# Kernel optimization log

Measured on AMD Instinct MI355X. Metric: run time of the kernel, lower is better.

## Reference

```python
import jax, jax.numpy as jnp
import numpy as np

N, P, Q, T, J, B, H = 262144, 64, 64, 2048, 512, 8, 64


def setup_inputs() -> dict:
    key = jax.random.key(0)
    ks = jax.random.split(key, 11)
    sH = 1.0 / np.sqrt(H).astype(np.float32)
    return {
        "idx": jax.random.randint(ks[0], (B,), 0, J),
        "seg_ids": jnp.sort(jax.random.randint(ks[1], (N,), 0, T)),
        "K": jax.random.normal(ks[2], (N, P), jnp.float32) * 0.1,
        "V": jax.random.normal(ks[3], (N, Q), jnp.float32),
        "S": jax.random.normal(ks[4], (P, J), jnp.float32) * 0.1,
        "W_ih": jax.random.normal(ks[5], (3 * H, Q), jnp.float32) * sH,
        "W_hh": jax.random.normal(ks[6], (3 * H, H), jnp.float32) * sH,
        "b_ih": jax.random.normal(ks[7], (3 * H,), jnp.float32) * sH,
        "b_hh": jax.random.normal(ks[8], (3 * H,), jnp.float32) * sH,
        "w_out": jax.random.normal(ks[9], (1, H), jnp.float32) * sH,
        "b_out": jax.random.normal(ks[10], (1,), jnp.float32) * sH,
    }


def reference(idx, seg_ids, K, V, S, W_ih, W_hh, b_ih, b_hh, w_out, b_out):
    # W[:, b] = K @ S[:, idx[b]]  -> [N, B]
    w = K @ S[:, idx]
    # ragged per-segment softmax over the N axis (segments = date windows)
    m = jax.ops.segment_max(w, seg_ids, num_segments=T)          # [T, B]
    e = jnp.exp(w - m[seg_ids])                                  # [N, B]
    denom = jax.ops.segment_sum(e, seg_ids, num_segments=T)     # [T, B]
    alpha = e / denom[seg_ids]                                   # [N, B]
    # weighted aggregation of V rows per segment: M[t, b] = sum_u alpha_u * V_u
    M = jax.ops.segment_sum(alpha[:, :, None] * V[:, None, :],
                            seg_ids, num_segments=T)             # [T, B, Q]
    X = jnp.transpose(M, (1, 0, 2))                              # [B, T, Q]

    # PyTorch GRU (gate order r,z,n). Faithful to the original bug: GRU was
    # built without batch_first=True, so axis 0 (B) is time, axis 1 (T) is batch.
    def step(h, x_t):  # x_t: [T, Q], h: [T, H]
        gi = x_t @ W_ih.T + b_ih                                 # [T, 3H]
        gh = h @ W_hh.T + b_hh                                   # [T, 3H]
        i_r, i_z, i_n = jnp.split(gi, 3, axis=1)
        h_r, h_z, h_n = jnp.split(gh, 3, axis=1)
        r = jax.nn.sigmoid(i_r + h_r)
        z = jax.nn.sigmoid(i_z + h_z)
        n = jnp.tanh(i_n + r * h_n)
        h_new = (1.0 - z) * n + z * h
        return h_new, h_new

    h0 = jnp.zeros((T, H), X.dtype)
    _, hs = jax.lax.scan(step, h0, X)                            # [B, T, H]
    preds = hs @ w_out.T + b_out                                 # [B, T, 1]
    return preds
```

## Files before the change

### kernel.cpp

```cpp
#include <hip/hip_runtime.h>
#include <math.h>

#define NN 262144
#define PP 64
#define QQ 64
#define TT 2048
#define JJ 512
#define BB 8
#define HH 64

__device__ __forceinline__ float lane_bcast(float v, int l) {
  return __int_as_float(__builtin_amdgcn_readlane(__float_as_int(v), l));
}

__global__ void k_prep(const int* __restrict__ seg_ids, const int* __restrict__ idx,
                       const float* __restrict__ S, int* __restrict__ seg_start,
                       float* __restrict__ s_cols) {
  int tid = blockIdx.x * blockDim.x + threadIdx.x;
  if (tid <= TT) {
    int lo = 0, hi = NN;
    while (lo < hi) {
      int mid = (lo + hi) >> 1;
      int v = seg_ids[mid];
      if (v < tid) lo = mid + 1; else hi = mid;
    }
    seg_start[tid] = lo;
  }
  int t2 = tid - (TT + 1);
  if (t2 >= 0 && t2 < PP * BB) {
    int p = t2 >> 3, b = t2 & 7;
    s_cols[b * PP + p] = S[p * JJ + idx[b]];
  }
}

__global__ __launch_bounds__(256) void k_w(const float* __restrict__ Kmat,
                                           const float* __restrict__ s_cols,
                                           float* __restrict__ ew) {
  __shared__ __align__(16) float s_lds[BB * PP];
  int tid = threadIdx.x;
  for (int i = tid; i < BB * PP; i += 256) s_lds[i] = s_cols[i];
  __syncthreads();
  int n = blockIdx.x * 64 + (tid >> 2);
  int sub = tid & 3;
  const float4* Kp = reinterpret_cast<const float4*>(Kmat + (size_t)n * PP + sub * 16);
  float4 kq[4];
#pragma unroll
  for (int j = 0; j < 4; ++j) kq[j] = Kp[j];
  float acc[8];
#pragma unroll
  for (int b = 0; b < 8; ++b) acc[b] = 0.f;
#pragma unroll
  for (int j4 = 0; j4 < 4; ++j4) {
    float4 kk = kq[j4];
#pragma unroll
    for (int b = 0; b < 8; ++b) {
      const float4 sv = *reinterpret_cast<const float4*>(&s_lds[b * PP + sub * 16 + j4 * 4]);
      acc[b] += kk.x * sv.x + kk.y * sv.y + kk.z * sv.z + kk.w * sv.w;
    }
  }
#pragma unroll
  for (int b = 0; b < 8; ++b) {
    acc[b] += __shfl_xor(acc[b], 1);
    acc[b] += __shfl_xor(acc[b], 2);
  }
  float ox = (sub == 0) ? acc[0] : (sub == 1) ? acc[2] : (sub == 2) ? acc[4] : acc[6];
  float oy = (sub == 0) ? acc[1] : (sub == 1) ? acc[3] : (sub == 2) ? acc[5] : acc[7];
  reinterpret_cast<float2*>(ew + (size_t)n * 8)[sub] =
      make_float2(__expf(ox), __expf(oy));
}

__global__ __launch_bounds__(256) void k_seg(const float* __restrict__ ew,
                                             const float* __restrict__ V,
                                             const int* __restrict__ seg_start,
                                             float* __restrict__ M) {
  int lane = threadIdx.x & 63, wv = threadIdx.x >> 6;
  int t = blockIdx.x * 4 + wv;
  int s = seg_start[t], e = seg_start[t + 1];
  int rsub = lane >> 4;
  int qg = lane & 15;

  float4 acc[8];
#pragma unroll
  for (int b = 0; b < 8; ++b) acc[b] = make_float4(0.f, 0.f, 0.f, 0.f);
  float4 selo = make_float4(0.f, 0.f, 0.f, 0.f);
  float4 sehi = make_float4(0.f, 0.f, 0.f, 0.f);

  int nq = (e - s + 3) >> 2;
  for (int i = 0; i < nq; ++i) {
    int r = s + i * 4 + rsub;
    if (r < e) {
      const float4* ewp = reinterpret_cast<const float4*>(ew + (size_t)r * 8);
      float4 elo = ewp[0], ehi = ewp[1];
      float4 vv = reinterpret_cast<const float4*>(V + (size_t)r * QQ)[qg];
      selo.x += elo.x; selo.y += elo.y; selo.z += elo.z; selo.w += elo.w;
      sehi.x += ehi.x; sehi.y += ehi.y; sehi.z += ehi.z; sehi.w += ehi.w;
      acc[0].x += elo.x * vv.x; acc[0].y += elo.x * vv.y; acc[0].z += elo.x * vv.z; acc[0].w += elo.x * vv.w;
      acc[1].x += elo.y * vv.x; acc[1].y += elo.y * vv.y; acc[1].z += elo.y * vv.z; acc[1].w += elo.y * vv.w;
      acc[2].x += elo.z * vv.x; acc[2].y += elo.z * vv.y; acc[2].z += elo.z * vv.z; acc[2].w += elo.z * vv.w;
      acc[3].x += elo.w * vv.x; acc[3].y += elo.w * vv.y; acc[3].z += elo.w * vv.z; acc[3].w += elo.w * vv.w;
      acc[4].x += ehi.x * vv.x; acc[4].y += ehi.x * vv.y; acc[4].z += ehi.x * vv.z; acc[4].w += ehi.x * vv.w;
      acc[5].x += ehi.y * vv.x; acc[5].y += ehi.y * vv.y; acc[5].z += ehi.y * vv.z; acc[5].w += ehi.y * vv.w;
      acc[6].x += ehi.z * vv.x; acc[6].y += ehi.z * vv.y; acc[6].z += ehi.z * vv.z; acc[6].w += ehi.z * vv.w;
      acc[7].x += ehi.w * vv.x; acc[7].y += ehi.w * vv.y; acc[7].z += ehi.w * vv.z; acc[7].w += ehi.w * vv.w;
    }
  }

#pragma unroll
  for (int b = 0; b < 8; ++b) {
    acc[b].x += __shfl_xor(acc[b].x, 16); acc[b].y += __shfl_xor(acc[b].y, 16);
    acc[b].z += __shfl_xor(acc[b].z, 16); acc[b].w += __shfl_xor(acc[b].w, 16);
    acc[b].x += __shfl_xor(acc[b].x, 32); acc[b].y += __shfl_xor(acc[b].y, 32);
    acc[b].z += __shfl_xor(acc[b].z, 32); acc[b].w += __shfl_xor(acc[b].w, 32);
  }
  selo.x += __shfl_xor(selo.x, 16); selo.y += __shfl_xor(selo.y, 16);
  selo.z += __shfl_xor(selo.z, 16); selo.w += __shfl_xor(selo.w, 16);
  sehi.x += __shfl_xor(sehi.x, 16); sehi.y += __shfl_xor(sehi.y, 16);
  sehi.z += __shfl_xor(sehi.z, 16); sehi.w += __shfl_xor(sehi.w, 16);
  selo.x += __shfl_xor(selo.x, 32); selo.y += __shfl_xor(selo.y, 32);
  selo.z += __shfl_xor(selo.z, 32); selo.w += __shfl_xor(selo.w, 32);
  sehi.x += __shfl_xor(sehi.x, 32); sehi.y += __shfl_xor(sehi.y, 32);
  sehi.z += __shfl_xor(sehi.z, 32); sehi.w += __shfl_xor(sehi.w, 32);

  if (rsub == 0) {
    float inv[8];
    inv[0] = (selo.x > 0.f) ? 1.f / selo.x : 0.f;
    inv[1] = (selo.y > 0.f) ? 1.f / selo.y : 0.f;
    inv[2] = (selo.z > 0.f) ? 1.f / selo.z : 0.f;
    inv[3] = (selo.w > 0.f) ? 1.f / selo.w : 0.f;
    inv[4] = (sehi.x > 0.f) ? 1.f / sehi.x : 0.f;
    inv[5] = (sehi.y > 0.f) ? 1.f / sehi.y : 0.f;
    inv[6] = (sehi.z > 0.f) ? 1.f / sehi.z : 0.f;
    inv[7] = (sehi.w > 0.f) ? 1.f / sehi.w : 0.f;
#pragma unroll
    for (int b = 0; b < 8; ++b) {
      float4 o = make_float4(acc[b].x * inv[b], acc[b].y * inv[b],
                             acc[b].z * inv[b], acc[b].w * inv[b]);
      *reinterpret_cast<float4*>(M + (size_t)t * 512 + b * 64 + qg * 4) = o;
    }
  }
}

__global__ __launch_bounds__(256) void k_gi(const float* __restrict__ M,
                                            const float* __restrict__ W_ih,
                                            const float* __restrict__ b_ih,
                                            float* __restrict__ GI) {
  __shared__ float Wt[64 * 193];
  int tid = threadIdx.x;
  for (int i = tid; i < 192 * 64; i += 256) {
    int g = i >> 6, k = i & 63;
    Wt[k * 193 + g] = W_ih[i];
  }
  __syncthreads();
  int lane = tid & 63, wv = tid >> 6;
  int row0 = blockIdx.x * 32 + wv * 8;
  float x[8];
#pragma unroll
  for (int rr = 0; rr < 8; ++rr) {
    int rho = row0 + rr;
    int b = rho >> 11, t = rho & 2047;
    x[rr] = M[((size_t)t * 8 + b) * 64 + lane];
  }
  float bi0 = b_ih[lane], bi1 = b_ih[64 + lane], bi2 = b_ih[128 + lane];
  float a0[8], a1[8], a2[8];
#pragma unroll
  for (int rr = 0; rr < 8; ++rr) { a0[rr] = bi0; a1[rr] = bi1; a2[rr] = bi2; }
#pragma unroll
  for (int k = 0; k < 64; ++k) {
    float w0 = Wt[k * 193 + lane];
    float w1 = Wt[k * 193 + 64 + lane];
    float w2 = Wt[k * 193 + 128 + lane];
#pragma unroll
    for (int rr = 0; rr < 8; ++rr) {
      float xk = lane_bcast(x[rr], k);
      a0[rr] += w0 * xk; a1[rr] += w1 * xk; a2[rr] += w2 * xk;
    }
  }
#pragma unroll
  for (int rr = 0; rr < 8; ++rr) {
    size_t rho = (size_t)row0 + rr;
    GI[rho * 192 + lane]       = a0[rr];
    GI[rho * 192 + 64 + lane]  = a1[rr];
    GI[rho * 192 + 128 + lane] = a2[rr];
  }
}

__global__ __launch_bounds__(256) void k_gru(const float* __restrict__ GI,
                                             const float* __restrict__ W_hh,
                                             const float* __restrict__ b_hh,
                                             const float* __restrict__ w_out,
                                             const float* __restrict__ b_out,
                                             float* __restrict__ preds) {
  __shared__ float Wt[64 * 193];
  int tid = threadIdx.x;
  for (int i = tid; i < 192 * 64; i += 256) {
    int g = i >> 6, k = i & 63;
    Wt[k * 193 + g] = W_hh[i];
  }
  __syncthreads();
  int lane = tid & 63, wv = tid >> 6;
  int t = blockIdx.x * 4 + wv;
  float bh0 = b_hh[lane], bh1 = b_hh[64 + lane], bh2 = b_hh[128 + lane];
  float wo = w_out[lane];
  float bo = b_out[0];

  float gr[8], gz[8], gn[8];
#pragma unroll
  for (int b = 0; b < 8; ++b) {
    size_t base = ((size_t)b * TT + t) * 192;
    gr[b] = GI[base + lane];
    gz[b] = GI[base + 64 + lane];
    gn[b] = GI[base + 128 + lane];
  }

  float h;
  {
    float r = 1.f / (1.f + __expf(-(gr[0] + bh0)));
    float z = 1.f / (1.f + __expf(-(gz[0] + bh1)));
    float nv = tanhf(gn[0] + r * bh2);
    h = (1.f - z) * nv;
    float pv = h * wo;
#pragma unroll
    for (int off = 32; off; off >>= 1) pv += __shfl_xor(pv, off);
    if (lane == 0) preds[t] = pv + bo;
  }
#pragma unroll
  for (int b = 1; b < 8; ++b) {
    float ar = bh0, az = bh1, an = bh2;
#pragma unroll
    for (int k = 0; k < 64; ++k) {
      float hk = lane_bcast(h, k);
      float w0 = Wt[k * 193 + lane];
      float w1 = Wt[k * 193 + 64 + lane];
      float w2 = Wt[k * 193 + 128 + lane];
      ar += w0 * hk; az += w1 * hk; an += w2 * hk;
    }
    float r = 1.f / (1.f + __expf(-(gr[b] + ar)));
    float z = 1.f / (1.f + __expf(-(gz[b] + az)));
    float nv = tanhf(gn[b] + r * an);
    h = (1.f - z) * nv + z * h;
    float pv = h * wo;
#pragma unroll
    for (int off = 32; off; off >>= 1) pv += __shfl_xor(pv, off);
    if (lane == 0) preds[(size_t)b * TT + t] = pv + bo;
  }
}

extern "C" void kernel_launch(void* const* d_in, const int* in_sizes, int n_in,
                              void* d_out, int out_size, void* d_ws, size_t ws_size,
                              hipStream_t stream) {
  const int*   idx     = (const int*)d_in[0];
  const int*   seg_ids = (const int*)d_in[1];
  const float* Kmat    = (const float*)d_in[2];
  const float* V       = (const float*)d_in[3];
  const float* S       = (const float*)d_in[4];
  const float* W_ih    = (const float*)d_in[5];
  const float* W_hh    = (const float*)d_in[6];
  const float* b_ih    = (const float*)d_in[7];
  const float* b_hh    = (const float*)d_in[8];
  const float* w_out   = (const float*)d_in[9];
  const float* b_out   = (const float*)d_in[10];
  float* out = (float*)d_out;

  char* ws = (char*)d_ws;
  int*   seg_start = (int*)(ws + 0);
  float* s_cols    = (float*)(ws + 8448);
  float* ew        = (float*)(ws + 10496);
  float* M         = (float*)(ws + 8399104);
  float* GI        = (float*)(ws + 12593408);

  hipLaunchKernelGGL(k_prep, dim3(11), dim3(256), 0, stream, seg_ids, idx, S, seg_start, s_cols);
  hipLaunchKernelGGL(k_w, dim3(NN / 64), dim3(256), 0, stream, Kmat, s_cols, ew);
  hipLaunchKernelGGL(k_seg, dim3(TT / 4), dim3(256), 0, stream, ew, V, seg_start, M);
  hipLaunchKernelGGL(k_gi, dim3(512), dim3(256), 0, stream, M, W_ih, b_ih, GI);
  hipLaunchKernelGGL(k_gru, dim3(512), dim3(256), 0, stream, GI, W_hh, b_hh, w_out, b_out, out);
}
```

Measured before the change: 80.54 us.

## Split segment aggregation across four waves per segment with separate reduction kernel

The segment-weighted V aggregation now gives each segment a whole block, with its four waves each handling a contiguous quarter of the segment's rows. Each wave writes unnormalized partial sums and partial softmax denominators to a scratch buffer. A new reduction kernel combines the four partials and normalizes into M. The aim is more parallelism and better load balance per segment, at the cost of an extra launch and a scratch buffer write and read (about 17 MB).

New measurement: 81.51 us. No clear change (+1.2%).

```diff
diff --git a/kernel.cpp b/kernel.cpp
--- a/kernel.cpp
+++ b/kernel.cpp
@@ -69,13 +69,19 @@
       make_float2(__expf(ox), __expf(oy));
 }
 
-__global__ __launch_bounds__(256) void k_seg(const float* __restrict__ ew,
-                                             const float* __restrict__ V,
-                                             const int* __restrict__ seg_start,
-                                             float* __restrict__ M) {
-  int lane = threadIdx.x & 63, wv = threadIdx.x >> 6;
-  int t = blockIdx.x * 4 + wv;
+#define PSTRIDE 520
+__global__ __launch_bounds__(256) void k_segp(const float* __restrict__ ew,
+                                              const float* __restrict__ V,
+                                              const int* __restrict__ seg_start,
+                                              float* __restrict__ P) {
+  int lane = threadIdx.x & 63, j = threadIdx.x >> 6;
+  int t = blockIdx.x;
   int s = seg_start[t], e = seg_start[t + 1];
+  int len = e - s;
+  int chunk = (len + 3) >> 2;
+  int b0 = s + j * chunk;
+  int b1 = b0 + chunk; if (b1 > e) b1 = e;
+  int slen = (b1 > b0) ? (b1 - b0) : 0;
   int rsub = lane >> 4;
   int qg = lane & 15;
 
@@ -85,25 +91,28 @@
   float4 selo = make_float4(0.f, 0.f, 0.f, 0.f);
   float4 sehi = make_float4(0.f, 0.f, 0.f, 0.f);
 
-  int nq = (e - s + 3) >> 2;
-  for (int i = 0; i < nq; ++i) {
-    int r = s + i * 4 + rsub;
-    if (r < e) {
-      const float4* ewp = reinterpret_cast<const float4*>(ew + (size_t)r * 8);
-      float4 elo = ewp[0], ehi = ewp[1];
-      float4 vv = reinterpret_cast<const float4*>(V + (size_t)r * QQ)[qg];
-      selo.x += elo.x; selo.y += elo.y; selo.z += elo.z; selo.w += elo.w;
-      sehi.x += ehi.x; sehi.y += ehi.y; sehi.z += ehi.z; sehi.w += ehi.w;
-      acc[0].x += elo.x * vv.x; acc[0].y += elo.x * vv.y; acc[0].z += elo.x * vv.z; acc[0].w += elo.x * vv.w;
-      acc[1].x += elo.y * vv.x; acc[1].y += elo.y * vv.y; acc[1].z += elo.y * vv.z; acc[1].w += elo.y * vv.w;
-      acc[2].x += elo.z * vv.x; acc[2].y += elo.z * vv.y; acc[2].z += elo.z * vv.z; acc[2].w += elo.z * vv.w;
-      acc[3].x += elo.w * vv.x; acc[3].y += elo.w * vv.y; acc[3].z += elo.w * vv.z; acc[3].w += elo.w * vv.w;
-      acc[4].x += ehi.x * vv.x; acc[4].y += ehi.x * vv.y; acc[4].z += ehi.x * vv.z; acc[4].w += ehi.x * vv.w;
-      acc[5].x += ehi.y * vv.x; acc[5].y += ehi.y * vv.y; acc[5].z += ehi.y * vv.z; acc[5].w += ehi.y * vv.w;
-      acc[6].x += ehi.z * vv.x; acc[6].y += ehi.z * vv.y; acc[6].z += ehi.z * vv.z; acc[6].w += ehi.z * vv.w;
-      acc[7].x += ehi.w * vv.x; acc[7].y += ehi.w * vv.y; acc[7].z += ehi.w * vv.z; acc[7].w += ehi.w * vv.w;
-    }
-  }
+#define PROC(RR)                                                                                           \
+  {                                                                                                        \
+    int r_ = (RR);                                                                                         \
+    const float4* ewp_ = reinterpret_cast<const float4*>(ew + (size_t)r_ * 8);                             \
+    float4 elo = ewp_[0], ehi = ewp_[1];                                                                   \
+    float4 vv = reinterpret_cast<const float4*>(V + (size_t)r_ * QQ)[qg];                                  \
+    selo.x += elo.x; selo.y += elo.y; selo.z += elo.z; selo.w += elo.w;                                    \
+    sehi.x += ehi.x; sehi.y += ehi.y; sehi.z += ehi.z; sehi.w += ehi.w;                                    \
+    acc[0].x += elo.x * vv.x; acc[0].y += elo.x * vv.y; acc[0].z += elo.x * vv.z; acc[0].w += elo.x * vv.w; \
+    acc[1].x += elo.y * vv.x; acc[1].y += elo.y * vv.y; acc[1].z += elo.y * vv.z; acc[1].w += elo.y * vv.w; \
+    acc[2].x += elo.z * vv.x; acc[2].y += elo.z * vv.y; acc[2].z += elo.z * vv.z; acc[2].w += elo.z * vv.w; \
+    acc[3].x += elo.w * vv.x; acc[3].y += elo.w * vv.y; acc[3].z += elo.w * vv.z; acc[3].w += elo.w * vv.w; \
+    acc[4].x += ehi.x * vv.x; acc[4].y += ehi.x * vv.y; acc[4].z += ehi.x * vv.z; acc[4].w += ehi.x * vv.w; \
+    acc[5].x += ehi.y * vv.x; acc[5].y += ehi.y * vv.y; acc[5].z += ehi.y * vv.z; acc[5].w += ehi.y * vv.w; \
+    acc[6].x += ehi.z * vv.x; acc[6].y += ehi.z * vv.y; acc[6].z += ehi.z * vv.z; acc[6].w += ehi.z * vv.w; \
+    acc[7].x += ehi.w * vv.x; acc[7].y += ehi.w * vv.y; acc[7].z += ehi.w * vv.z; acc[7].w += ehi.w * vv.w; \
+  }
+
+  int nfull = slen >> 2, tail = slen & 3;
+  for (int i = 0; i < nfull; ++i) PROC(b0 + i * 4 + rsub);
+  if (tail && rsub < tail) PROC(b0 + nfull * 4 + rsub);
+#undef PROC
 
 #pragma unroll
   for (int b = 0; b < 8; ++b) {
@@ -121,23 +130,35 @@
   sehi.x += __shfl_xor(sehi.x, 32); sehi.y += __shfl_xor(sehi.y, 32);
   sehi.z += __shfl_xor(sehi.z, 32); sehi.w += __shfl_xor(sehi.w, 32);
 
+  float* Pp = P + ((size_t)t * 4 + j) * PSTRIDE;
   if (rsub == 0) {
-    float inv[8];
-    inv[0] = (selo.x > 0.f) ? 1.f / selo.x : 0.f;
-    inv[1] = (selo.y > 0.f) ? 1.f / selo.y : 0.f;
-    inv[2] = (selo.z > 0.f) ? 1.f / selo.z : 0.f;
-    inv[3] = (selo.w > 0.f) ? 1.f / selo.w : 0.f;
-    inv[4] = (sehi.x > 0.f) ? 1.f / sehi.x : 0.f;
-    inv[5] = (sehi.y > 0.f) ? 1.f / sehi.y : 0.f;
-    inv[6] = (sehi.z > 0.f) ? 1.f / sehi.z : 0.f;
-    inv[7] = (sehi.w > 0.f) ? 1.f / sehi.w : 0.f;
-#pragma unroll
-    for (int b = 0; b < 8; ++b) {
-      float4 o = make_float4(acc[b].x * inv[b], acc[b].y * inv[b],
-                             acc[b].z * inv[b], acc[b].w * inv[b]);
-      *reinterpret_cast<float4*>(M + (size_t)t * 512 + b * 64 + qg * 4) = o;
-    }
-  }
+#pragma unroll
+    for (int b = 0; b < 8; ++b)
+      *reinterpret_cast<float4*>(Pp + b * 64 + qg * 4) = acc[b];
+    if (qg == 0) {
+      Pp[512] = selo.x; Pp[513] = selo.y; Pp[514] = selo.z; Pp[515] = selo.w;
+      Pp[516] = sehi.x; Pp[517] = sehi.y; Pp[518] = sehi.z; Pp[519] = sehi.w;
+    }
+  }
+}
+
+__global__ __launch_bounds__(256) void k_red(const float* __restrict__ P,
+                                             float* __restrict__ M) {
+  __shared__ float se[32];
+  int t = blockIdx.x, tid = threadIdx.x;
+  if (tid < 32) se[tid] = P[((size_t)t * 4 + (tid >> 3)) * PSTRIDE + 512 + (tid & 7)];
+  __syncthreads();
+  int o = tid * 2;
+  int b = o >> 6;
+  float dd = se[b] + se[8 + b] + se[16 + b] + se[24 + b];
+  float inv = (dd > 0.f) ? 1.f / dd : 0.f;
+  float sx = 0.f, sy = 0.f;
+#pragma unroll
+  for (int j = 0; j < 4; ++j) {
+    float2 p = *reinterpret_cast<const float2*>(P + ((size_t)t * 4 + j) * PSTRIDE + o);
+    sx += p.x; sy += p.y;
+  }
+  *reinterpret_cast<float2*>(M + (size_t)t * 512 + o) = make_float2(sx * inv, sy * inv);
 }
 
 __global__ __launch_bounds__(256) void k_gi(const float* __restrict__ M,
@@ -267,10 +288,12 @@
   float* ew        = (float*)(ws + 10496);
   float* M         = (float*)(ws + 8399104);
   float* GI        = (float*)(ws + 12593408);
+  float* P         = (float*)(ws + 25176320);
 
   hipLaunchKernelGGL(k_prep, dim3(11), dim3(256), 0, stream, seg_ids, idx, S, seg_start, s_cols);
   hipLaunchKernelGGL(k_w, dim3(NN / 64), dim3(256), 0, stream, Kmat, s_cols, ew);
-  hipLaunchKernelGGL(k_seg, dim3(TT / 4), dim3(256), 0, stream, ew, V, seg_start, M);
+  hipLaunchKernelGGL(k_segp, dim3(TT), dim3(256), 0, stream, ew, V, seg_start, P);
+  hipLaunchKernelGGL(k_red, dim3(TT), dim3(256), 0, stream, P, M);
   hipLaunchKernelGGL(k_gi, dim3(512), dim3(256), 0, stream, M, W_ih, b_ih, GI);
   hipLaunchKernelGGL(k_gru, dim3(512), dim3(256), 0, stream, GI, W_hh, b_hh, w_out, b_out, out);
 }
```
